# Kernel optimization log

Measured on AMD Instinct MI355X. Metric: run time of the kernel, lower is better.

The kernel has to match this reference:

```python
import jax, jax.numpy as jnp
import numpy as np

B, H, S, D = 2, 16, 2048, 64
DEGREE = 2
EPS = 1e-4


def setup_inputs() -> dict:
    key = jax.random.key(0)
    kq, kk, kv = jax.random.split(key, 3)
    q = jax.random.normal(kq, (B, H, S, D), dtype=jnp.float32)
    k = jax.random.normal(kk, (B, H, S, D), dtype=jnp.float32)
    v = jax.random.normal(kv, (B, H, S, D), dtype=jnp.float32)
    return {"q": q, "k": k, "v": v}


def reference(q, k, v):
    # dots: [B,H,S,S] = QK^T
    dots = jnp.einsum("bhsd,bhtd->bhst", q, k)
    # polynomial kernel: x^degree, row-normalized with clamped denom
    x = dots ** DEGREE
    denom = jnp.maximum(x.sum(axis=-1, keepdims=True), EPS)
    attn = x / denom
    # weighted V sum: [B,H,S,D]
    return jnp.einsum("bhst,bhtd->bhsd", attn, v)
```

## Files before the change

### kernel.cpp

```cpp
#include <hip/hip_runtime.h>


#define S_LEN 2048
#define DH    64
#define BQ    64
#define BK    64
#define EPSTR 68
#define PSTR  65
#define BH_N  32
#define PER_BH (S_LEN * DH)
#define NT    (S_LEN / BK)

typedef __bf16 bf16x8 __attribute__((ext_vector_type(8)));
typedef __bf16 bf16x2 __attribute__((ext_vector_type(2)));
typedef float  f32x2  __attribute__((ext_vector_type(2)));
typedef float  f32x4  __attribute__((ext_vector_type(4)));
typedef float  f32x16 __attribute__((ext_vector_type(16)));
typedef unsigned int uivec2 __attribute__((ext_vector_type(2)));

__device__ __forceinline__ unsigned short f2bf(float f) {
    union { float f; unsigned int u; } x; x.f = f;
    unsigned int u = x.u;
    return (unsigned short)((u + 0x7fffu + ((u >> 16) & 1u)) >> 16);
}

__device__ __forceinline__ unsigned int pack2bf(float lo, float hi) {
#if __has_builtin(__builtin_amdgcn_cvt_pk_bf16_f32)
    bf16x2 p = __builtin_amdgcn_cvt_pk_bf16_f32(lo, hi);
    union { bf16x2 v; unsigned int u; } c; c.v = p;
    return c.u;
#else
    return (unsigned int)f2bf(lo) | ((unsigned int)f2bf(hi) << 16);
#endif
}

__device__ __forceinline__ void pl32swap(unsigned int& a, unsigned int& b) {
#if __has_builtin(__builtin_amdgcn_permlane32_swap)
    uivec2 r = __builtin_amdgcn_permlane32_swap(a, b, false, false);
    a = r[0]; b = r[1];
#else
    asm("v_permlane32_swap_b32 %0, %1" : "+v"(a), "+v"(b));
#endif
}

__global__ __launch_bounds__(256)
void prepass_kernel(const float* __restrict__ kg, const float* __restrict__ vg,
                    unsigned short* __restrict__ kfo, unsigned short* __restrict__ vfo)
{
    __shared__ unsigned short Lk[64 * 72];
    __shared__ unsigned short Lv[64 * PSTR];
    const int tid = threadIdx.x;
    const int bh  = blockIdx.y;
    const int t   = blockIdx.x;
    const size_t base = (size_t)bh * PER_BH + (size_t)t * 64 * DH;

    const float4* kf4 = (const float4*)(kg + base);
    const float4* vf4 = (const float4*)(vg + base);
    #pragma unroll
    for (int r = 0; r < 4; ++r) {
        int idx = r * 256 + tid;
        int row = idx >> 4, c4 = idx & 15;
        float4 f = kf4[idx];
        ushort4 hh;
        hh.x = f2bf(f.x); hh.y = f2bf(f.y); hh.z = f2bf(f.z); hh.w = f2bf(f.w);
        *(ushort4*)&Lk[row * 72 + c4 * 4] = hh;
        float4 g = vf4[idx];
        unsigned short* pv = &Lv[row * PSTR + c4 * 4];
        pv[0] = f2bf(g.x); pv[1] = f2bf(g.y); pv[2] = f2bf(g.z); pv[3] = f2bf(g.w);
    }
    __syncthreads();

    unsigned short* kout = kfo + (size_t)bh * PER_BH + (size_t)t * 4096;
    #pragma unroll
    for (int r = 0; r < 2; ++r) {
        int pos = r * 256 + tid;
        int lam = pos & 63, rest = pos >> 6;
        int e = rest >> 2, ks = rest & 3;
        int l31 = lam & 31, h = lam >> 5;
        uint4 v = *(const uint4*)&Lk[(e * 32 + l31) * 72 + ks * 16 + h * 8];
        *(uint4*)(kout + (size_t)pos * 8) = v;
    }
    unsigned short* vout = vfo + (size_t)bh * PER_BH + (size_t)t * 4096;
    #pragma unroll
    for (int r = 0; r < 2; ++r) {
        int pos = r * 256 + tid;
        int lam = pos & 63, rest = pos >> 6;
        int e = rest >> 2, ksl = (rest >> 1) & 1, mt = rest & 1;
        int l31 = lam & 31, h = lam >> 5;
        int d  = mt * 32 + l31;
        int j0 = e * 32 + ksl * 16 + h * 8;
        union { unsigned short s[8]; uint4 u; } u;
        #pragma unroll
        for (int jj = 0; jj < 8; ++jj) u.s[jj] = Lv[(j0 + jj) * PSTR + d];
        *(uint4*)(vout + (size_t)pos * 8) = u.u;
    }
}

__global__ __launch_bounds__(256, 4)
void poly_attn_main(const float* __restrict__ qg,
                    const unsigned short* __restrict__ kfo,
                    const unsigned short* __restrict__ vfo,
                    float* __restrict__ og)
{
    __shared__ float epb[4 * 32 * EPSTR];
    __shared__ float dbuf[128];

    const int tid  = threadIdx.x;
    const int lane = tid & 63;
    const int w    = tid >> 6;
    const int sp   = w >> 1;
    const int e    = w & 1;
    const int l31  = lane & 31;
    const int h    = lane >> 5;

    const int id = blockIdx.x;
    const int r5 = id & 31;
    const int bh = (r5 & 7) * 4 + (r5 >> 3);
    const int qt = id >> 5;
    const int q0 = qt * BQ;

    const float* qb = qg + ((size_t)bh * S_LEN + q0) * DH;
    const unsigned short* kw = kfo + (size_t)bh * PER_BH + e * 2048 + (size_t)lane * 8;
    const unsigned short* vw = vfo + (size_t)bh * PER_BH + e * 2048 + (size_t)lane * 8;
    float* ob = og + ((size_t)bh * S_LEN + q0) * DH;

    bf16x8 qfrag[4];
    #pragma unroll
    for (int ks = 0; ks < 4; ++ks) {
        const float* qp = qb + (32 * sp + l31) * DH + ks * 16 + h * 8;
        float4 f0 = *(const float4*)qp;
        float4 f1 = *(const float4*)(qp + 4);
        union { unsigned int d[4]; bf16x8 v; } u;
        u.d[0] = pack2bf(f0.x, f0.y);
        u.d[1] = pack2bf(f0.z, f0.w);
        u.d[2] = pack2bf(f1.x, f1.y);
        u.d[3] = pack2bf(f1.z, f1.w);
        qfrag[ks] = u.v;
    }

    f32x16 oacc[2];
    #pragma unroll
    for (int mt = 0; mt < 2; ++mt)
        #pragma unroll
        for (int r = 0; r < 16; ++r) oacc[mt][r] = 0.f;
    f32x2 ds2; ds2[0] = 0.f; ds2[1] = 0.f;

    uint4 kbuf[4], vbuf[4];
    unsigned int bsave[2][4];

    const unsigned short* kload = kw;
    const unsigned short* vload = vw;
    #pragma unroll
    for (int x = 0; x < 4; ++x) kbuf[x] = *(const uint4*)(kload + x * 512);
    kload += 4096;

#define KLOAD()                                                                     \
        { _Pragma("unroll")                                                         \
          for (int x = 0; x < 4; ++x) kbuf[x] = *(const uint4*)(kload + x * 512);   \
          kload += 4096; }

#define VLOAD()                                                                     \
        { _Pragma("unroll")                                                         \
          for (int x = 0; x < 4; ++x) vbuf[x] = *(const uint4*)(vload + x * 512);   \
          vload += 4096; }

#define QK_STAGE()                                                                  \
        f32x16 acc;                                                                 \
        _Pragma("unroll")                                                           \
        for (int r = 0; r < 16; ++r) acc[r] = 0.f;                                  \
        _Pragma("unroll")                                                           \
        for (int ks = 0; ks < 4; ++ks) {                                            \
            union { uint4 u; bf16x8 v; } kc; kc.u = kbuf[ks];                       \
            acc = __builtin_amdgcn_mfma_f32_32x32x16_bf16(kc.v, qfrag[ks], acc, 0, 0, 0); \
        }

#define PV_STAGE()                                                                  \
        _Pragma("unroll")                                                           \
        for (int ksl = 0; ksl < 2; ++ksl) {                                         \
            union { unsigned int d[4]; bf16x8 v; } bu;                              \
            bu.d[0] = bsave[ksl][0]; bu.d[1] = bsave[ksl][1];                       \
            bu.d[2] = bsave[ksl][2]; bu.d[3] = bsave[ksl][3];                       \
            _Pragma("unroll")                                                       \
            for (int mt = 0; mt < 2; ++mt) {                                        \
                union { uint4 u; bf16x8 v; } vv; vv.u = vbuf[ksl * 2 + mt];         \
                oacc[mt] = __builtin_amdgcn_mfma_f32_32x32x16_bf16(vv.v, bu.v, oacc[mt], 0, 0, 0); \
            }                                                                       \
        }

#define XF_STAGE()                                                                  \
        _Pragma("unroll")                                                           \
        for (int ksl = 0; ksl < 2; ++ksl) {                                         \
            f32x2 va, vb, vc, vd;                                                   \
            va[0] = acc[8*ksl+0]; va[1] = acc[8*ksl+1];                             \
            vb[0] = acc[8*ksl+2]; vb[1] = acc[8*ksl+3];                             \
            vc[0] = acc[8*ksl+4]; vc[1] = acc[8*ksl+5];                             \
            vd[0] = acc[8*ksl+6]; vd[1] = acc[8*ksl+7];                             \
            va = va * va; vb = vb * vb; vc = vc * vc; vd = vd * vd;                 \
            ds2 += va; ds2 += vb; ds2 += vc; ds2 += vd;                             \
            unsigned int a0 = pack2bf(va[0], va[1]);                                \
            unsigned int a1 = pack2bf(vb[0], vb[1]);                                \
            unsigned int b0 = pack2bf(vc[0], vc[1]);                                \
            unsigned int b1 = pack2bf(vd[0], vd[1]);                                \
            pl32swap(a0, b0);                                                       \
            pl32swap(a1, b1);                                                       \
            bsave[ksl][0] = a0; bsave[ksl][1] = a1;                                 \
            bsave[ksl][2] = b0; bsave[ksl][3] = b1;                                 \
        }

    { QK_STAGE(); KLOAD(); XF_STAGE(); }

    for (int T = 1; T < NT - 1; ++T) {
        VLOAD();
        QK_STAGE();
        KLOAD();
        PV_STAGE();
        XF_STAGE();
    }
    { VLOAD(); QK_STAGE(); PV_STAGE(); XF_STAGE(); }
    { VLOAD(); PV_STAGE(); }
#undef KLOAD
#undef VLOAD
#undef QK_STAGE
#undef PV_STAGE
#undef XF_STAGE

    float wavetot;
    { float t = ds2[0] + ds2[1]; wavetot = t + __shfl_xor(t, 32); }

    {
        float* ep = epb + (size_t)w * (32 * EPSTR);
        #pragma unroll
        for (int mt = 0; mt < 2; ++mt) {
            #pragma unroll
            for (int g = 0; g < 4; ++g) {
                f32x4 vv;
                vv[0] = oacc[mt][4*g+0];
                vv[1] = oacc[mt][4*g+1];
                vv[2] = oacc[mt][4*g+2];
                vv[3] = oacc[mt][4*g+3];
                *(f32x4*)&ep[l31 * EPSTR + mt * 32 + 8 * g + 4 * h] = vv;
            }
        }
        if (h == 0) dbuf[w * 32 + l31] = wavetot;
    }
    __syncthreads();

    const int so = w >> 1, ho = w & 1;
    const int lr = lane >> 1;
    const float den = dbuf[(2 * so + 0) * 32 + lr] + dbuf[(2 * so + 1) * 32 + lr];
    const float inv = 1.0f / fmaxf(den, 1e-4f);
    const float* ea = epb + (size_t)(2 * so + 0) * (32 * EPSTR) + lr * EPSTR;
    const float* eb = epb + (size_t)(2 * so + 1) * (32 * EPSTR) + lr * EPSTR;
    #pragma unroll
    for (int it = 0; it < 4; ++it) {
        int d0 = ho * 32 + (lane & 1) * 16 + it * 4;
        f32x4 a = *(const f32x4*)&ea[d0];
        f32x4 b = *(const f32x4*)&eb[d0];
        f32x4 sm;
        sm[0] = (a[0] + b[0]) * inv;
        sm[1] = (a[1] + b[1]) * inv;
        sm[2] = (a[2] + b[2]) * inv;
        sm[3] = (a[3] + b[3]) * inv;
        *(f32x4*)&ob[(32 * so + lr) * DH + d0] = sm;
    }
}

#define LSTR 72
__global__ __launch_bounds__(256, 2)
void poly_attn_fallback(const float* __restrict__ qg, const float* __restrict__ kg,
                        const float* __restrict__ vg, float* __restrict__ og)
{
    __shared__ unsigned short Qs[64 * LSTR];
    __shared__ unsigned short Ksl[64 * LSTR];
    __shared__ unsigned short Vt[64 * LSTR];
    __shared__ unsigned short Xsl[64 * LSTR];

    const int tid  = threadIdx.x;
    const int lane = tid & 63;
    const int w    = tid >> 6;
    const int c    = lane & 15;
    const int quad = lane >> 4;
    const int i0   = w * 16;

    const int bh = blockIdx.y;
    const int q0 = blockIdx.x * 64;

    const float* qb = qg + ((size_t)bh * S_LEN + q0) * DH;
    const float* kb = kg + (size_t)bh * S_LEN * DH;
    const float* vb = vg + (size_t)bh * S_LEN * DH;
    float*       ob = og + ((size_t)bh * S_LEN + q0) * DH;

    {
        const float4* qf4 = (const float4*)qb;
        #pragma unroll
        for (int r = 0; r < 4; ++r) {
            int idx = r * 256 + tid;
            int row = idx >> 4, c4 = idx & 15;
            float4 f = qf4[idx];
            ushort4 hh;
            hh.x = f2bf(f.x); hh.y = f2bf(f.y); hh.z = f2bf(f.z); hh.w = f2bf(f.w);
            *(ushort4*)&Qs[row * LSTR + c4 * 4] = hh;
        }
    }

    f32x4 oacc[4];
    #pragma unroll
    for (int t = 0; t < 4; ++t) { oacc[t][0]=0.f; oacc[t][1]=0.f; oacc[t][2]=0.f; oacc[t][3]=0.f; }
    float dsum[4] = {0.f, 0.f, 0.f, 0.f};

    for (int t0 = 0; t0 < S_LEN; t0 += 64) {
        __syncthreads();
        {
            const float4* kf4 = (const float4*)(kb + (size_t)t0 * DH);
            const float4* vf4 = (const float4*)(vb + (size_t)t0 * DH);
            #pragma unroll
            for (int r = 0; r < 4; ++r) {
                int idx = r * 256 + tid;
                int row = idx >> 4, c4 = idx & 15;
                float4 f = kf4[idx];
                ushort4 hh;
                hh.x = f2bf(f.x); hh.y = f2bf(f.y); hh.z = f2bf(f.z); hh.w = f2bf(f.w);
                *(ushort4*)&Ksl[row * LSTR + c4 * 4] = hh;
                float4 g = vf4[idx];
                int d0 = c4 * 4;
                Vt[(d0 + 0) * LSTR + row] = f2bf(g.x);
                Vt[(d0 + 1) * LSTR + row] = f2bf(g.y);
                Vt[(d0 + 2) * LSTR + row] = f2bf(g.z);
                Vt[(d0 + 3) * LSTR + row] = f2bf(g.w);
            }
        }
        __syncthreads();

        f32x4 xacc[4];
        #pragma unroll
        for (int t = 0; t < 4; ++t) { xacc[t][0]=0.f; xacc[t][1]=0.f; xacc[t][2]=0.f; xacc[t][3]=0.f; }
        #pragma unroll
        for (int k0 = 0; k0 < 64; k0 += 32) {
            bf16x8 af = *(const bf16x8*)&Qs[(i0 + c) * LSTR + k0 + quad * 8];
            #pragma unroll
            for (int tn = 0; tn < 4; ++tn) {
                bf16x8 bfg = *(const bf16x8*)&Ksl[(tn * 16 + c) * LSTR + k0 + quad * 8];
                xacc[tn] = __builtin_amdgcn_mfma_f32_16x16x32_bf16(af, bfg, xacc[tn], 0, 0, 0);
            }
        }
        #pragma unroll
        for (int tn = 0; tn < 4; ++tn)
            #pragma unroll
            for (int r = 0; r < 4; ++r) {
                float xv = xacc[tn][r];
                float xs = xv * xv;
                dsum[r] += xs;
                Xsl[(i0 + quad * 4 + r) * LSTR + tn * 16 + c] = f2bf(xs);
            }
        __syncthreads();

        #pragma unroll
        for (int k0 = 0; k0 < 64; k0 += 32) {
            bf16x8 af = *(const bf16x8*)&Xsl[(i0 + c) * LSTR + k0 + quad * 8];
            #pragma unroll
            for (int tn = 0; tn < 4; ++tn) {
                bf16x8 bfg = *(const bf16x8*)&Vt[(tn * 16 + c) * LSTR + k0 + quad * 8];
                oacc[tn] = __builtin_amdgcn_mfma_f32_16x16x32_bf16(af, bfg, oacc[tn], 0, 0, 0);
            }
        }
    }

    #pragma unroll
    for (int r = 0; r < 4; ++r) {
        float s = dsum[r];
        s += __shfl_xor(s, 1);
        s += __shfl_xor(s, 2);
        s += __shfl_xor(s, 4);
        s += __shfl_xor(s, 8);
        dsum[r] = 1.0f / fmaxf(s, 1e-4f);
    }
    #pragma unroll
    for (int tn = 0; tn < 4; ++tn)
        #pragma unroll
        for (int r = 0; r < 4; ++r)
            ob[(i0 + quad * 4 + r) * DH + tn * 16 + c] = oacc[tn][r] * dsum[r];
}

extern "C" void kernel_launch(void* const* d_in, const int* in_sizes, int n_in,
                              void* d_out, int out_size, void* d_ws, size_t ws_size,
                              hipStream_t stream) {
    (void)in_sizes; (void)n_in; (void)out_size;
    const float* q = (const float*)d_in[0];
    const float* k = (const float*)d_in[1];
    const float* v = (const float*)d_in[2];
    float* o = (float*)d_out;

    const size_t elems = (size_t)BH_N * PER_BH;
    const size_t need  = 2 * elems * sizeof(unsigned short);

    if (ws_size >= need) {
        unsigned short* kfo = (unsigned short*)d_ws;
        unsigned short* vfo = kfo + elems;
        prepass_kernel<<<dim3(NT, BH_N), 256, 0, stream>>>(k, v, kfo, vfo);
        poly_attn_main<<<dim3(BH_N * S_LEN / BQ), 256, 0, stream>>>(q, kfo, vfo, o);
    } else {
        poly_attn_fallback<<<dim3(S_LEN / 64, BH_N), 256, 0, stream>>>(q, k, v, o);
    }
}
```

Before: 139.8 us.

## Stage K/V tiles through LDS with async global_load_lds double buffering

Replaces per-wave register loads of K and V fragments with a cooperative double-buffered LDS pipeline. Each of the four waves issues direct global-to-LDS DMA for one quarter of the next K/V tile while all waves compute on the current tile. This halves redundant global traffic, since the two sp waves previously loaded the same K/V, and overlaps the loads with compute. In exchange it adds two workgroup barriers per tile and LDS reads, and the QK and PV work of each tile is no longer software-pipelined across iterations.

New measurement: 142.2 us. About the same (+1.7%).

```diff
diff --git a/kernel.cpp b/kernel.cpp
--- a/kernel.cpp
+++ b/kernel.cpp
@@ -10,6 +10,7 @@
 #define BH_N  32
 #define PER_BH (S_LEN * DH)
 #define NT    (S_LEN / BK)
+#define SMEM_BYTES 35328
 
 typedef __bf16 bf16x8 __attribute__((ext_vector_type(8)));
 typedef __bf16 bf16x2 __attribute__((ext_vector_type(2)));
@@ -41,6 +42,12 @@
 #else
     asm("v_permlane32_swap_b32 %0, %1" : "+v"(a), "+v"(b));
 #endif
+}
+
+__device__ __forceinline__ void dma16(const void* g, void* l) {
+    __builtin_amdgcn_global_load_lds(
+        (const __attribute__((address_space(1))) unsigned int*)g,
+        (__attribute__((address_space(3))) unsigned int*)l, 16, 0, 0);
 }
 
 __global__ __launch_bounds__(256)
@@ -102,8 +109,7 @@
                     const unsigned short* __restrict__ vfo,
                     float* __restrict__ og)
 {
-    __shared__ float epb[4 * 32 * EPSTR];
-    __shared__ float dbuf[128];
+    __shared__ __align__(16) unsigned char smem[SMEM_BYTES];
 
     const int tid  = threadIdx.x;
     const int lane = tid & 63;
@@ -120,9 +126,20 @@
     const int q0 = qt * BQ;
 
     const float* qb = qg + ((size_t)bh * S_LEN + q0) * DH;
-    const unsigned short* kw = kfo + (size_t)bh * PER_BH + e * 2048 + (size_t)lane * 8;
-    const unsigned short* vw = vfo + (size_t)bh * PER_BH + e * 2048 + (size_t)lane * 8;
+    const unsigned short* kt = kfo + (size_t)bh * PER_BH;
+    const unsigned short* vt = vfo + (size_t)bh * PER_BH;
     float* ob = og + ((size_t)bh * S_LEN + q0) * DH;
+
+    const unsigned short* gsrc_base =
+        (w < 2) ? (kt + (size_t)w * 2048 + (size_t)lane * 8)
+                : (vt + (size_t)(w - 2) * 2048 + (size_t)lane * 8);
+
+    {
+        unsigned char* lb = smem + (size_t)w * 4096;
+        #pragma unroll
+        for (int i = 0; i < 4; ++i)
+            dma16(gsrc_base + i * 512, lb + i * 1024);
+    }
 
     bf16x8 qfrag[4];
     #pragma unroll
@@ -145,47 +162,7 @@
         for (int r = 0; r < 16; ++r) oacc[mt][r] = 0.f;
     f32x2 ds2; ds2[0] = 0.f; ds2[1] = 0.f;
 
-    uint4 kbuf[4], vbuf[4];
-    unsigned int bsave[2][4];
-
-    const unsigned short* kload = kw;
-    const unsigned short* vload = vw;
-    #pragma unroll
-    for (int x = 0; x < 4; ++x) kbuf[x] = *(const uint4*)(kload + x * 512);
-    kload += 4096;
-
-#define KLOAD()                                                                     \
-        { _Pragma("unroll")                                                         \
-          for (int x = 0; x < 4; ++x) kbuf[x] = *(const uint4*)(kload + x * 512);   \
-          kload += 4096; }
-
-#define VLOAD()                                                                     \
-        { _Pragma("unroll")                                                         \
-          for (int x = 0; x < 4; ++x) vbuf[x] = *(const uint4*)(vload + x * 512);   \
-          vload += 4096; }
-
-#define QK_STAGE()                                                                  \
-        f32x16 acc;                                                                 \
-        _Pragma("unroll")                                                           \
-        for (int r = 0; r < 16; ++r) acc[r] = 0.f;                                  \
-        _Pragma("unroll")                                                           \
-        for (int ks = 0; ks < 4; ++ks) {                                            \
-            union { uint4 u; bf16x8 v; } kc; kc.u = kbuf[ks];                       \
-            acc = __builtin_amdgcn_mfma_f32_32x32x16_bf16(kc.v, qfrag[ks], acc, 0, 0, 0); \
-        }
-
-#define PV_STAGE()                                                                  \
-        _Pragma("unroll")                                                           \
-        for (int ksl = 0; ksl < 2; ++ksl) {                                         \
-            union { unsigned int d[4]; bf16x8 v; } bu;                              \
-            bu.d[0] = bsave[ksl][0]; bu.d[1] = bsave[ksl][1];                       \
-            bu.d[2] = bsave[ksl][2]; bu.d[3] = bsave[ksl][3];                       \
-            _Pragma("unroll")                                                       \
-            for (int mt = 0; mt < 2; ++mt) {                                        \
-                union { uint4 u; bf16x8 v; } vv; vv.u = vbuf[ksl * 2 + mt];         \
-                oacc[mt] = __builtin_amdgcn_mfma_f32_32x32x16_bf16(vv.v, bu.v, oacc[mt], 0, 0, 0); \
-            }                                                                       \
-        }
+    unsigned int bsv[2][4];
 
 #define XF_STAGE()                                                                  \
         _Pragma("unroll")                                                           \
@@ -203,30 +180,76 @@
             unsigned int b1 = pack2bf(vd[0], vd[1]);                                \
             pl32swap(a0, b0);                                                       \
             pl32swap(a1, b1);                                                       \
-            bsave[ksl][0] = a0; bsave[ksl][1] = a1;                                 \
-            bsave[ksl][2] = b0; bsave[ksl][3] = b1;                                 \
-        }
-
-    { QK_STAGE(); KLOAD(); XF_STAGE(); }
-
-    for (int T = 1; T < NT - 1; ++T) {
-        VLOAD();
-        QK_STAGE();
-        KLOAD();
-        PV_STAGE();
-        XF_STAGE();
-    }
-    { VLOAD(); QK_STAGE(); PV_STAGE(); XF_STAGE(); }
-    { VLOAD(); PV_STAGE(); }
-#undef KLOAD
-#undef VLOAD
-#undef QK_STAGE
-#undef PV_STAGE
+            bsv[ksl][0] = a0; bsv[ksl][1] = a1;                                     \
+            bsv[ksl][2] = b0; bsv[ksl][3] = b1;                                     \
+        }
+
+#define STEP(TT, CUR, PF)                                                           \
+    {                                                                               \
+        if (PF) {                                                                   \
+            const unsigned short* gs_ = gsrc_base + (size_t)((TT) + 1) * 4096;      \
+            unsigned char* lb_ = smem + ((CUR) ^ 1) * 16384 + (size_t)w * 4096;     \
+            _Pragma("unroll")                                                       \
+            for (int i = 0; i < 4; ++i)                                             \
+                dma16(gs_ + i * 512, lb_ + i * 1024);                               \
+            asm volatile("s_waitcnt vmcnt(4)" ::: "memory");                        \
+        } else {                                                                    \
+            asm volatile("s_waitcnt vmcnt(0)" ::: "memory");                        \
+        }                                                                           \
+        __builtin_amdgcn_s_barrier();                                               \
+        asm volatile("" ::: "memory");                                              \
+        __builtin_amdgcn_sched_barrier(0);                                          \
+        const unsigned char* cb_ = smem + (CUR) * 16384;                            \
+        const unsigned char* kb_ = cb_ + e * 4096 + (size_t)lane * 16;              \
+        uint4 kf0 = *(const uint4*)(kb_);                                           \
+        uint4 kf1 = *(const uint4*)(kb_ + 1024);                                    \
+        uint4 kf2 = *(const uint4*)(kb_ + 2048);                                    \
+        uint4 kf3 = *(const uint4*)(kb_ + 3072);                                    \
+        f32x16 acc;                                                                 \
+        _Pragma("unroll")                                                           \
+        for (int r = 0; r < 16; ++r) acc[r] = 0.f;                                  \
+        {                                                                           \
+            union { uint4 u; bf16x8 v; } kc;                                        \
+            kc.u = kf0; acc = __builtin_amdgcn_mfma_f32_32x32x16_bf16(kc.v, qfrag[0], acc, 0, 0, 0); \
+            kc.u = kf1; acc = __builtin_amdgcn_mfma_f32_32x32x16_bf16(kc.v, qfrag[1], acc, 0, 0, 0); \
+            kc.u = kf2; acc = __builtin_amdgcn_mfma_f32_32x32x16_bf16(kc.v, qfrag[2], acc, 0, 0, 0); \
+            kc.u = kf3; acc = __builtin_amdgcn_mfma_f32_32x32x16_bf16(kc.v, qfrag[3], acc, 0, 0, 0); \
+        }                                                                           \
+        const unsigned char* vb_ = cb_ + 8192 + e * 4096 + (size_t)lane * 16;       \
+        uint4 vf0 = *(const uint4*)(vb_);                                           \
+        uint4 vf1 = *(const uint4*)(vb_ + 1024);                                    \
+        uint4 vf2 = *(const uint4*)(vb_ + 2048);                                    \
+        uint4 vf3 = *(const uint4*)(vb_ + 3072);                                    \
+        XF_STAGE();                                                                 \
+        _Pragma("unroll")                                                           \
+        for (int ksl = 0; ksl < 2; ++ksl) {                                         \
+            union { unsigned int d[4]; bf16x8 v; } bu;                              \
+            bu.d[0] = bsv[ksl][0]; bu.d[1] = bsv[ksl][1];                           \
+            bu.d[2] = bsv[ksl][2]; bu.d[3] = bsv[ksl][3];                           \
+            union { uint4 u; bf16x8 v; } vv;                                        \
+            vv.u = (ksl == 0 ? vf0 : vf2);                                          \
+            oacc[0] = __builtin_amdgcn_mfma_f32_32x32x16_bf16(vv.v, bu.v, oacc[0], 0, 0, 0); \
+            vv.u = (ksl == 0 ? vf1 : vf3);                                          \
+            oacc[1] = __builtin_amdgcn_mfma_f32_32x32x16_bf16(vv.v, bu.v, oacc[1], 0, 0, 0); \
+        }                                                                           \
+        __builtin_amdgcn_s_barrier();                                               \
+        asm volatile("" ::: "memory");                                              \
+    }
+
+    for (int T = 0; T < NT - 2; T += 2) {
+        STEP(T,     0, 1);
+        STEP(T + 1, 1, 1);
+    }
+    STEP(NT - 2, 0, 1);
+    STEP(NT - 1, 1, 0);
+#undef STEP
 #undef XF_STAGE
 
     float wavetot;
     { float t = ds2[0] + ds2[1]; wavetot = t + __shfl_xor(t, 32); }
 
+    float* epb  = (float*)smem;
+    float* dbuf = (float*)(smem + 34816);
     {
         float* ep = epb + (size_t)w * (32 * EPSTR);
         #pragma unroll
```

## Restructure main loop with K double-buffering, MFMA row-sum, and setprio

Applied to the files above, without the earlier changes.

Reorganizes the per-tile loop into a body with double-buffered K registers, where each tile's V load is issued at the start of that tile rather than overlapped with the previous QK stage. The row-sum of squared scores is now computed on the matrix cores with an extra MFMA against a vector of bf16 ones, replacing the VALU accumulation and the cross-lane shuffle. MFMA sections are wrapped in s_setprio. Launch bounds drop to 3 blocks per SM to give more registers. Together these aim to cut VALU work and improve overlap, at the cost of an extra MFMA per step and lower occupancy. The denominator now sums bf16-rounded values, which slightly changes numerics.

Result: slower. 143.1 us (+2.4%).

```diff
diff --git a/kernel.cpp b/kernel.cpp
--- a/kernel.cpp
+++ b/kernel.cpp
@@ -96,7 +96,7 @@
     }
 }
 
-__global__ __launch_bounds__(256, 4)
+__global__ __launch_bounds__(256, 3)
 void poly_attn_main(const float* __restrict__ qg,
                     const unsigned short* __restrict__ kfo,
                     const unsigned short* __restrict__ vfo,
@@ -143,51 +143,56 @@
     for (int mt = 0; mt < 2; ++mt)
         #pragma unroll
         for (int r = 0; r < 16; ++r) oacc[mt][r] = 0.f;
-    f32x2 ds2; ds2[0] = 0.f; ds2[1] = 0.f;
-
-    uint4 kbuf[4], vbuf[4];
-    unsigned int bsave[2][4];
-
-    const unsigned short* kload = kw;
-    const unsigned short* vload = vw;
-    #pragma unroll
-    for (int x = 0; x < 4; ++x) kbuf[x] = *(const uint4*)(kload + x * 512);
-    kload += 4096;
-
-#define KLOAD()                                                                     \
-        { _Pragma("unroll")                                                         \
-          for (int x = 0; x < 4; ++x) kbuf[x] = *(const uint4*)(kload + x * 512);   \
-          kload += 4096; }
-
-#define VLOAD()                                                                     \
-        { _Pragma("unroll")                                                         \
-          for (int x = 0; x < 4; ++x) vbuf[x] = *(const uint4*)(vload + x * 512);   \
-          vload += 4096; }
-
-#define QK_STAGE()                                                                  \
+    f32x16 oaccD;
+    #pragma unroll
+    for (int r = 0; r < 16; ++r) oaccD[r] = 0.f;
+
+    f32x16 zacc;
+    #pragma unroll
+    for (int r = 0; r < 16; ++r) zacc[r] = 0.f;
+    asm volatile("" : "+v"(zacc));
+
+    bf16x8 onesv;
+    {
+        union { unsigned int d[4]; bf16x8 v; } u;
+        u.d[0] = 0x3f803f80u; u.d[1] = 0x3f803f80u;
+        u.d[2] = 0x3f803f80u; u.d[3] = 0x3f803f80u;
+        onesv = u.v;
+    }
+    asm volatile("" : "+v"(onesv));
+
+    uint4 kbuf[2][4], vbuf[4];
+    unsigned int bsv[2][4];
+
+    #pragma unroll
+    for (int x = 0; x < 4; ++x) kbuf[0][x] = *(const uint4*)(kw + x * 512);
+
+#define BODY(TT, CUR, NXT, KPF)                                                     \
+    {                                                                               \
+        {                                                                           \
+            const unsigned short* vn_ = vw + (size_t)(TT) * 4096;                   \
+            _Pragma("unroll")                                                       \
+            for (int x = 0; x < 4; ++x) vbuf[x] = *(const uint4*)(vn_ + x * 512);   \
+        }                                                                           \
         f32x16 acc;                                                                 \
-        _Pragma("unroll")                                                           \
-        for (int r = 0; r < 16; ++r) acc[r] = 0.f;                                  \
-        _Pragma("unroll")                                                           \
-        for (int ks = 0; ks < 4; ++ks) {                                            \
-            union { uint4 u; bf16x8 v; } kc; kc.u = kbuf[ks];                       \
-            acc = __builtin_amdgcn_mfma_f32_32x32x16_bf16(kc.v, qfrag[ks], acc, 0, 0, 0); \
-        }
-
-#define PV_STAGE()                                                                  \
-        _Pragma("unroll")                                                           \
-        for (int ksl = 0; ksl < 2; ++ksl) {                                         \
-            union { unsigned int d[4]; bf16x8 v; } bu;                              \
-            bu.d[0] = bsave[ksl][0]; bu.d[1] = bsave[ksl][1];                       \
-            bu.d[2] = bsave[ksl][2]; bu.d[3] = bsave[ksl][3];                       \
+        __builtin_amdgcn_s_setprio(1);                                              \
+        {                                                                           \
+            union { uint4 u; bf16x8 v; } kc;                                        \
+            kc.u = kbuf[CUR][0];                                                    \
+            acc = __builtin_amdgcn_mfma_f32_32x32x16_bf16(kc.v, qfrag[0], zacc, 0, 0, 0); \
+            kc.u = kbuf[CUR][1];                                                    \
+            acc = __builtin_amdgcn_mfma_f32_32x32x16_bf16(kc.v, qfrag[1], acc, 0, 0, 0); \
+            kc.u = kbuf[CUR][2];                                                    \
+            acc = __builtin_amdgcn_mfma_f32_32x32x16_bf16(kc.v, qfrag[2], acc, 0, 0, 0); \
+            kc.u = kbuf[CUR][3];                                                    \
+            acc = __builtin_amdgcn_mfma_f32_32x32x16_bf16(kc.v, qfrag[3], acc, 0, 0, 0); \
+        }                                                                           \
+        __builtin_amdgcn_s_setprio(0);                                              \
+        if (KPF) {                                                                  \
+            const unsigned short* kn_ = kw + (size_t)((TT) + 1) * 4096;             \
             _Pragma("unroll")                                                       \
-            for (int mt = 0; mt < 2; ++mt) {                                        \
-                union { uint4 u; bf16x8 v; } vv; vv.u = vbuf[ksl * 2 + mt];         \
-                oacc[mt] = __builtin_amdgcn_mfma_f32_32x32x16_bf16(vv.v, bu.v, oacc[mt], 0, 0, 0); \
-            }                                                                       \
-        }
-
-#define XF_STAGE()                                                                  \
+            for (int x = 0; x < 4; ++x) kbuf[NXT][x] = *(const uint4*)(kn_ + x * 512); \
+        }                                                                           \
         _Pragma("unroll")                                                           \
         for (int ksl = 0; ksl < 2; ++ksl) {                                         \
             f32x2 va, vb, vc, vd;                                                   \
@@ -196,36 +201,40 @@
             vc[0] = acc[8*ksl+4]; vc[1] = acc[8*ksl+5];                             \
             vd[0] = acc[8*ksl+6]; vd[1] = acc[8*ksl+7];                             \
             va = va * va; vb = vb * vb; vc = vc * vc; vd = vd * vd;                 \
-            ds2 += va; ds2 += vb; ds2 += vc; ds2 += vd;                             \
             unsigned int a0 = pack2bf(va[0], va[1]);                                \
             unsigned int a1 = pack2bf(vb[0], vb[1]);                                \
             unsigned int b0 = pack2bf(vc[0], vc[1]);                                \
             unsigned int b1 = pack2bf(vd[0], vd[1]);                                \
             pl32swap(a0, b0);                                                       \
             pl32swap(a1, b1);                                                       \
-            bsave[ksl][0] = a0; bsave[ksl][1] = a1;                                 \
-            bsave[ksl][2] = b0; bsave[ksl][3] = b1;                                 \
-        }
-
-    { QK_STAGE(); KLOAD(); XF_STAGE(); }
-
-    for (int T = 1; T < NT - 1; ++T) {
-        VLOAD();
-        QK_STAGE();
-        KLOAD();
-        PV_STAGE();
-        XF_STAGE();
-    }
-    { VLOAD(); QK_STAGE(); PV_STAGE(); XF_STAGE(); }
-    { VLOAD(); PV_STAGE(); }
-#undef KLOAD
-#undef VLOAD
-#undef QK_STAGE
-#undef PV_STAGE
-#undef XF_STAGE
-
-    float wavetot;
-    { float t = ds2[0] + ds2[1]; wavetot = t + __shfl_xor(t, 32); }
+            bsv[ksl][0] = a0; bsv[ksl][1] = a1;                                     \
+            bsv[ksl][2] = b0; bsv[ksl][3] = b1;                                     \
+        }                                                                           \
+        __builtin_amdgcn_s_setprio(1);                                              \
+        _Pragma("unroll")                                                           \
+        for (int ksl = 0; ksl < 2; ++ksl) {                                         \
+            union { unsigned int d[4]; bf16x8 v; } bu;                              \
+            bu.d[0] = bsv[ksl][0]; bu.d[1] = bsv[ksl][1];                           \
+            bu.d[2] = bsv[ksl][2]; bu.d[3] = bsv[ksl][3];                           \
+            union { uint4 u; bf16x8 v; } vv;                                        \
+            vv.u = vbuf[ksl * 2 + 0];                                               \
+            oacc[0] = __builtin_amdgcn_mfma_f32_32x32x16_bf16(vv.v, bu.v, oacc[0], 0, 0, 0); \
+            vv.u = vbuf[ksl * 2 + 1];                                               \
+            oacc[1] = __builtin_amdgcn_mfma_f32_32x32x16_bf16(vv.v, bu.v, oacc[1], 0, 0, 0); \
+            oaccD  = __builtin_amdgcn_mfma_f32_32x32x16_bf16(onesv, bu.v, oaccD, 0, 0, 0); \
+        }                                                                           \
+        __builtin_amdgcn_s_setprio(0);                                              \
+    }
+
+    for (int T = 0; T < NT - 2; T += 2) {
+        BODY(T,     0, 1, 1);
+        BODY(T + 1, 1, 0, 1);
+    }
+    BODY(NT - 2, 0, 1, 1);
+    BODY(NT - 1, 1, 0, 0);
+#undef BODY
+
+    const float wavetot = oaccD[0];
 
     {
         float* ep = epb + (size_t)w * (32 * EPSTR);
```
